# Optimization experiments

Hardware: AMD Instinct MI355X
Metric: run time of the kernel (lower is better)

## Reference

```python
import jax, jax.numpy as jnp
from jax import lax
import numpy as np

B, IMG_H, IMG_W = 8, 256, 512
NUM_CLASSES, P = 20, 32
SCALE, TOPK, IOU_THR = 32.0, 100, 0.5


def conv2d(x, w, b, stride=1, pad=1):
    y = lax.conv_general_dilated(x, w, (stride, stride), [(pad, pad), (pad, pad)],
                                 dimension_numbers=('NCHW', 'OIHW', 'NCHW'))
    return y + b[None, :, None, None]


def bilinear_resize(img, out_h, out_w):
    # img: [..., H, W]; torch F.interpolate(mode='bilinear', align_corners=False)
    H, W = img.shape[-2], img.shape[-1]
    def idx_w(n_in, n_out):
        src = (jnp.arange(n_out, dtype=jnp.float32) + 0.5) * (n_in / n_out) - 0.5
        src = jnp.clip(src, 0.0, n_in - 1)
        i0 = jnp.floor(src).astype(jnp.int32)
        i1 = jnp.minimum(i0 + 1, n_in - 1)
        return i0, i1, src - i0.astype(jnp.float32)
    y0, y1, wy = idx_w(H, out_h)
    x0, x1, wx = idx_w(W, out_w)
    top = img[..., y0, :] * (1.0 - wy)[:, None] + img[..., y1, :] * wy[:, None]
    return top[..., x0] * (1.0 - wx) + top[..., x1] * wx


def generate_anchors(fh, fw):
    ys = (jnp.arange(fh, dtype=jnp.float32) + 0.5) * (IMG_H / fh)
    xs = (jnp.arange(fw, dtype=jnp.float32) + 0.5) * (IMG_W / fw)
    cy, cx = jnp.meshgrid(ys, xs, indexing='ij')
    h = SCALE / 2
    return jnp.stack([cx - h, cy - h, cx + h, cy + h], -1).reshape(-1, 4)


def delta_to_boxes(anchors, deltas):
    a_c = (anchors[:, :2] + anchors[:, 2:]) / 2
    a_wh = anchors[:, 2:] - anchors[:, :2]
    pc = a_c + deltas[..., :2] * a_wh
    pwh = a_wh * jnp.exp(deltas[..., 2:])
    return jnp.concatenate([pc - pwh / 2, pc + pwh / 2], -1)


def nms_single(boxes, scores, labels):
    # torchvision batched_nms: offset boxes per label, greedy NMS, return kept idxs
    N = boxes.shape[0]
    off = labels.astype(boxes.dtype) * (jnp.max(boxes) + 1.0)
    b = boxes + off[:, None]
    order = jnp.argsort(-scores)
    bs = b[order]
    area = (bs[:, 2] - bs[:, 0]) * (bs[:, 3] - bs[:, 1])
    lt = jnp.maximum(bs[:, None, :2], bs[None, :, :2])
    rb = jnp.minimum(bs[:, None, 2:], bs[None, :, 2:])
    wh = jnp.clip(rb - lt, 0.0)
    inter = wh[..., 0] * wh[..., 1]
    iou = inter / (area[:, None] + area[None, :] - inter + 1e-9)
    idxs = jnp.arange(N)
    def body(i, suppressed):
        keep_i = jnp.logical_not(suppressed[i])
        row = (iou[i] > IOU_THR) & (idxs > i)
        return jnp.where(keep_i, suppressed | row, suppressed)
    suppressed = lax.fori_loop(0, N, body, jnp.zeros(N, bool))
    keep_mask = ~suppressed
    rank = jnp.cumsum(keep_mask) - 1
    slots = jnp.where(keep_mask & (rank < TOPK), rank, TOPK)
    out = jnp.full(TOPK + 1, -1, jnp.int32).at[slots].set(order.astype(jnp.int32))
    return out[:TOPK]


def setup_inputs():
    key = jax.random.key(0)
    ks = jax.random.split(key, 17)
    def cw(k, o, i, kh, kw_):
        return jax.random.normal(k, (o, i, kh, kw_), jnp.float32) / np.sqrt(i * kh * kw_)
    return {
        'images': jax.random.normal(ks[0], (B, 3, IMG_H, IMG_W), jnp.float32),
        'w1': cw(ks[1], 64, 3, 3, 3),   'b1': jnp.zeros(64, jnp.float32),
        'w2': cw(ks[2], 128, 64, 3, 3), 'b2': jnp.zeros(128, jnp.float32),
        'w3': cw(ks[3], 256, 128, 3, 3),'b3': jnp.zeros(256, jnp.float32),
        'pw1': cw(ks[4], 256, 256, 3, 3), 'pb1': jnp.zeros(256, jnp.float32),
        'pw2': cw(ks[5], P, 256, 1, 1),   'pb2': jnp.zeros(P, jnp.float32),
        'cw_': cw(ks[6], NUM_CLASSES + 1, 256, 3, 3), 'cb': jnp.zeros(NUM_CLASSES + 1, jnp.float32),
        'bw': cw(ks[7], 4, 256, 3, 3),  'bb': jnp.zeros(4, jnp.float32),
        'kw': cw(ks[8], P, 256, 3, 3),  'kb': jnp.zeros(P, jnp.float32),
    }


def reference(images, w1, b1, w2, b2, w3, b3, pw1, pb1, pw2, pb2, cw_, cb, bw, bb, kw, kb):
    x = jax.nn.relu(conv2d(images, w1, b1, stride=2))
    x = jax.nn.relu(conv2d(x, w2, b2, stride=2))
    feat = jax.nn.relu(conv2d(x, w3, b3, stride=2))          # [B,256,32,64]
    proto = conv2d(jax.nn.relu(conv2d(feat, pw1, pb1)), pw2, pb2, pad=0)  # [B,P,32,64]
    fh, fw = feat.shape[2], feat.shape[3]
    def head(w, b, c):
        return conv2d(feat, w, b).transpose(0, 2, 3, 1).reshape(B, -1, c)
    cls = head(cw_, cb, NUM_CLASSES + 1)     # [B,N,C+1]
    box = head(bw, bb, 4)                    # [B,N,4]
    coef = head(kw, kb, P)                   # [B,N,P]
    anchors = generate_anchors(fh, fw)       # [N,4]
    probs = jax.nn.softmax(cls, -1)[..., :-1]
    scores = probs.max(-1)
    labels = probs.argmax(-1).astype(jnp.int32)
    boxes = delta_to_boxes(anchors, box)     # [B,N,4]
    keep = jax.vmap(nms_single)(boxes, scores, labels)   # [B,100], -1 pad
    valid = keep >= 0
    ki = jnp.clip(keep, 0)
    take = lambda a: jnp.take_along_axis(a, ki[..., None] if a.ndim == 3 else ki, axis=1)
    boxes_k = take(boxes) * valid[..., None]
    scores_k = take(scores) * valid
    labels_k = jnp.where(valid, take(labels), 0)
    coef_k = jnp.take_along_axis(coef, ki[..., None], axis=1)   # [B,100,P]
    m = jax.nn.sigmoid(jnp.einsum('bkp,bphw->bkhw', coef_k, proto))
    masks = bilinear_resize(m, IMG_H, IMG_W) > 0.5
    masks = masks & valid[..., None, None]
    return boxes_k, scores_k, labels_k, masks, valid
```

## Files before the change

kernel.cpp:

```cpp
#include <hip/hip_runtime.h>
#include <hip/hip_bf16.h>
#include <math.h>

#define BB 8
#define NCLS 21
#define NANCH 2048
#define TOPK_N 100

static const size_t OFF_X1HI = 0;
static const size_t OFF_X1LO = 34344960;
static const size_t OFF_X2HI = 68689920;
static const size_t OFF_X2LO = 86261760;
static const size_t OFF_FTHI = 103833600;
static const size_t OFF_FTLO = 113025024;
static const size_t OFF_WT1  = 122216448;
static const size_t OFF_A2H  = 122223616;
static const size_t OFF_A2L  = 122371072;
static const size_t OFF_A3H  = 122518528;
static const size_t OFF_A3L  = 123108352;
static const size_t OFF_AHH  = 123698176;
static const size_t OFF_AHL  = 123993088;
static const size_t OFF_AP1H = 124288000;
static const size_t OFF_AP1L = 125467648;
static const size_t OFF_WTP2 = 126647296;
static const size_t OFF_BH   = 126680064;
static const size_t OFF_HOUT = 126680576;
static const size_t OFF_P1   = 130874880;
static const size_t OFF_PROTO= 147652096;
static const size_t OFF_BOXES= 149749248;
static const size_t OFF_SCORES=150011392;
static const size_t OFF_LABELS=150076928;
static const size_t OFF_ORDER= 150142464;
static const size_t OFF_SB   = 150208000;
static const size_t OFF_IOU  = 150470144;
static const size_t OFF_KEEP = 154664448;
static const size_t OFF_MAXB = 154668032;

static const size_t OUT_BOXES  = 0;
static const size_t OUT_SCORES = 3200;
static const size_t OUT_LABELS = 4000;
static const size_t OUT_MASKS  = 4800;
static const size_t OUT_VALID  = 104862400;

typedef __attribute__((ext_vector_type(8))) short bf16x8;
typedef __attribute__((ext_vector_type(4))) float f32x4;

__device__ __forceinline__ unsigned encf(float f){
  unsigned u = __float_as_uint(f);
  return (u & 0x80000000u) ? ~u : (u | 0x80000000u);
}
__device__ __forceinline__ float decf(unsigned u){
  unsigned b = (u & 0x80000000u) ? (u & 0x7fffffffu) : ~u;
  return __uint_as_float(b);
}
__device__ __forceinline__ short f2bf(float f){
  __hip_bfloat16 h = __float2bfloat16(f);
  return *(short*)&h;
}
__device__ __forceinline__ float bf2f(short h){
  return __uint_as_float(((unsigned)(unsigned short)h) << 16);
}

__global__ void halok3(short* __restrict__ x1hi, short* __restrict__ x1lo,
                       short* __restrict__ x2hi, short* __restrict__ x2lo,
                       short* __restrict__ fthi, short* __restrict__ ftlo,
                       unsigned* __restrict__ maxb){
  int i = blockIdx.x*256 + threadIdx.x;
  if (i < BB) maxb[i] = 0u;
  short *hi, *lo; int Hp, Wp, cell, bg;
  if (i < 49408){
    hi=x1hi; lo=x1lo; Hp=130; Wp=258; cell = i % 772; bg = i / 772;
  } else if (i < 99072){
    int j = i - 49408; hi=x2hi; lo=x2lo; Hp=66; Wp=130; cell = j % 388; bg = j / 388;
  } else if (i < 149248){
    int j = i - 99072; hi=fthi; lo=ftlo; Hp=34; Wp=66; cell = j % 196; bg = j / 196;
  } else return;
  int y, x;
  if (cell < Wp)        { y = 0;      x = cell; }
  else if (cell < 2*Wp) { y = Hp-1;   x = cell - Wp; }
  else { int r = cell - 2*Wp; y = 1 + (r>>1); x = (r&1) ? (Wp-1) : 0; }
  size_t ad = (((size_t)bg*Hp + y)*Wp + x)*8;
  bf16x8 z = (bf16x8){0,0,0,0,0,0,0,0};
  *(bf16x8*)(hi + ad) = z;
  *(bf16x8*)(lo + ad) = z;
}

template<int CIN,int COUT,int KK>
__device__ __forceinline__ void packw_body(int i, const float* __restrict__ w,
                                           float* __restrict__ wT){
  if (i >= CIN*KK*COUT) return;
  int co = i % COUT; int r = i / COUT;
  int ci = r / KK,  k = r % KK;
  wT[i] = w[(co*CIN + ci)*KK + k];
}

template<int CIN,int COUT>
__device__ __forceinline__ void packA_body(int i, const float* __restrict__ w,
                                           short* __restrict__ Ahi, short* __restrict__ Alo){
  constexpr int K = CIN*9;
  constexpr int KS = K/32;
  if (i >= COUT*K) return;
  int sub  = i & 7;
  int lane = (i >> 3) & 63;
  int rest = i >> 9;
  int ks = rest % KS;
  int mt = rest / KS;
  int m = mt*16 + (lane & 15);
  int k = ks*32 + (lane >> 4)*8 + sub;
  int tap = k / CIN, ci = k - tap*CIN;
  float v = w[(m*CIN + ci)*9 + tap];
  short h = f2bf(v);
  Ahi[i] = h;
  Alo[i] = f2bf(v - bf2f(h));
}

__device__ __forceinline__ void packAh_body(int i,
    const float* __restrict__ cw, const float* __restrict__ bw,
    const float* __restrict__ kw, const float* __restrict__ cb,
    const float* __restrict__ bb, const float* __restrict__ kb,
    short* __restrict__ Ahi, short* __restrict__ Alo, float* __restrict__ bh){
  if (i < 64){
    float v = 0.f;
    if (i < 21) v = cb[i]; else if (i < 25) v = bb[i-21]; else if (i < 57) v = kb[i-25];
    bh[i] = v;
  }
  if (i >= 64*2304) return;
  constexpr int KS = 72;
  int sub  = i & 7;
  int lane = (i >> 3) & 63;
  int rest = i >> 9;
  int ks = rest % KS;
  int mt = rest / KS;
  int m = mt*16 + (lane & 15);
  int k = ks*32 + (lane >> 4)*8 + sub;
  int tap = k >> 8, ci = k & 255;
  float v = 0.f;
  if (m < 21)      v = cw[(m*256 + ci)*9 + tap];
  else if (m < 25) v = bw[((m-21)*256 + ci)*9 + tap];
  else if (m < 57) v = kw[((m-25)*256 + ci)*9 + tap];
  short h = f2bf(v);
  Ahi[i] = h;
  Alo[i] = f2bf(v - bf2f(h));
}

__global__ void packall(const float* __restrict__ w1, float* __restrict__ wT1,
                        const float* __restrict__ w2, short* __restrict__ a2h, short* __restrict__ a2l,
                        const float* __restrict__ w3, short* __restrict__ a3h, short* __restrict__ a3l,
                        const float* __restrict__ pw1, short* __restrict__ ap1h, short* __restrict__ ap1l,
                        const float* __restrict__ cw, const float* __restrict__ bw,
                        const float* __restrict__ kw, const float* __restrict__ cb,
                        const float* __restrict__ bb, const float* __restrict__ kb,
                        short* __restrict__ ahh, short* __restrict__ ahl, float* __restrict__ bh,
                        const float* __restrict__ pw2, float* __restrict__ wTp2){
  int blk = blockIdx.x, t = threadIdx.x;
  if (blk < 288)        packA_body<64,128>(blk*256+t, w2, a2h, a2l);
  else if (blk < 1440)  packA_body<128,256>((blk-288)*256+t, w3, a3h, a3l);
  else if (blk < 3744)  packA_body<256,256>((blk-1440)*256+t, pw1, ap1h, ap1l);
  else if (blk < 4320)  packAh_body((blk-3744)*256+t, cw,bw,kw,cb,bb,kb, ahh,ahl,bh);
  else if (blk < 4327)  packw_body<3,64,9>((blk-4320)*256+t, w1, wT1);
  else                  packw_body<256,32,1>((blk-4327)*256+t, pw2, wTp2);
}

__global__ __launch_bounds__(256) void conv1k(const float* __restrict__ img,
    const float* __restrict__ wT, const float* __restrict__ bias,
    short* __restrict__ x1hi, short* __restrict__ x1lo){
  const int b   = blockIdx.z;
  const int co0 = blockIdx.y * 16;
  const int g   = blockIdx.x*256 + threadIdx.x;
  const int y  = g >> 7;
  const int x0 = (g & 127) << 1;

  float acc[16][2];
#pragma unroll
  for (int c=0;c<16;c++){
    float bv = bias[co0+c];
    acc[c][0] = bv; acc[c][1] = bv;
  }
  int   off[3][5];
  float msk[3][5];
#pragma unroll
  for (int kh=0;kh<3;kh++){
    int iy = y*2 - 1 + kh;
    bool okr = (iy >= 0) && (iy < 256);
    int ro = okr ? iy*512 : 0;
#pragma unroll
    for (int t=0;t<5;t++){
      int col = x0*2 - 1 + t;
      bool ok = okr && (col >= 0) && (col < 512);
      off[kh][t] = ok ? (ro + col) : 0;
      msk[kh][t] = ok ? 1.f : 0.f;
    }
  }
  const float* inb = img + (size_t)b*3*256*512;
  for (int ci=0; ci<3; ci++){
    const float* inc = inb + (size_t)ci*256*512;
    float v[3][5];
#pragma unroll
    for (int kh=0;kh<3;kh++)
#pragma unroll
      for (int t=0;t<5;t++)
        v[kh][t] = inc[off[kh][t]] * msk[kh][t];
    const float* wp = wT + ci*9*64 + co0;
#pragma unroll
    for (int kh=0;kh<3;kh++)
#pragma unroll
    for (int kw=0;kw<3;kw++){
      const float* wq = wp + (kh*3+kw)*64;
#pragma unroll
      for (int c=0;c<16;c++){
        float wv = wq[c];
        acc[c][0] = fmaf(wv, v[kh][2*0+kw], acc[c][0]);
        acc[c][1] = fmaf(wv, v[kh][2*1+kw], acc[c][1]);
      }
    }
  }
#pragma unroll
  for (int s=0;s<2;s++){
    short hv[16] __attribute__((aligned(16)));
    short lv[16] __attribute__((aligned(16)));
#pragma unroll
    for (int c=0;c<16;c++){
      float r = fmaxf(acc[c][s], 0.f);
      short h = f2bf(r);
      hv[c] = h;
      lv[c] = f2bf(r - bf2f(h));
    }
#pragma unroll
    for (int g2=0; g2<2; g2++){
      size_t ad = (((size_t)(b*8 + (co0>>3) + g2)*130 + (y+1))*258 + (x0+s+1))*8;
      *(bf16x8*)(x1hi + ad) = *(bf16x8*)(hv + g2*8);
      *(bf16x8*)(x1lo + ad) = *(bf16x8*)(lv + g2*8);
    }
  }
}

template<int CIN,int K,int M,int MW,int NW,int S,int IPH,int IPW,int NXB,
         bool SPLIT,bool STAGELO,int EMODE,int OPH,int OPW>
__global__ __launch_bounds__(NW*64) void cgemm_row(
    const short* __restrict__ Ahi, const short* __restrict__ Alo,
    const short* __restrict__ Bhi, const short* __restrict__ Blo,
    const float* __restrict__ bias, float* __restrict__ outf,
    short* __restrict__ outhi, short* __restrict__ outlo){
  static_assert(CIN % 32 == 0, "CIN must be multiple of 32");
  constexpr int NT = 64*32;
  constexpr int KS = K/32;
  constexpr int CG = CIN/8;
  constexpr int SW  = 64*S + 2;
  constexpr int SWP = (S==2) ? (SW/2 + 1) : SW;
  constexpr int PARS = (S==2) ? 2 : 1;
  constexpr int LOOFF = CG*PARS*SWP*8;
  constexpr int BUFS = (SPLIT && STAGELO) ? 2 : 1;
  __shared__ __align__(16) short sB[BUFS*LOOFF];

  const int b    = blockIdx.z;
  const int oy   = blockIdx.x / NXB;
  const int xb   = (blockIdx.x % NXB) * 64;
  const int wave = threadIdx.x >> 6;
  const int lane = threadIdx.x & 63;
  const int lm = lane & 15, lq = lane >> 4;
  const int m0 = (blockIdx.y * NW + wave) * (MW*16);
  const int tid = threadIdx.x;

  f32x4 acc[MW][4];
#pragma unroll
  for (int i=0;i<MW;i++)
#pragma unroll
    for (int j=0;j<4;j++) acc[i][j] = (f32x4){0.f,0.f,0.f,0.f};

  const short* Ah_l = Ahi + (size_t)lane*8;
  const short* Al_l = Alo + (size_t)lane*8;
  const int mt0 = m0 >> 4;
  const size_t plane = (size_t)IPH*IPW;
  const short* Bl0 = Blo + ((size_t)b*CG + lq)*plane*8;

#pragma unroll 1
  for (int dy=0; dy<3; dy++){
    const int iy = oy*S + dy;
    __syncthreads();
    {
      const short* srch = Bhi + (((size_t)b*CG*IPH + iy)*IPW + (size_t)(xb*S))*8;
      for (int c = tid; c < CG*SW; c += NW*64){
        int g = c / SW, p = c - g*SW;
        int dst = (S==2) ? ((g*2 + (p&1))*SWP + (p>>1)) : (g*SW + p);
        *(bf16x8*)(&sB[(size_t)dst*8]) =
          *(const bf16x8*)(srch + ((size_t)g*plane + p)*8);
      }
      if constexpr (SPLIT && STAGELO){
        const short* srcl = Blo + (((size_t)b*CG*IPH + iy)*IPW + (size_t)(xb*S))*8;
        for (int c = tid; c < CG*SW; c += NW*64){
          int g = c / SW, p = c - g*SW;
          int dst = (S==2) ? ((g*2 + (p&1))*SWP + (p>>1)) : (g*SW + p);
          *(bf16x8*)(&sB[LOOFF + (size_t)dst*8]) =
            *(const bf16x8*)(srcl + ((size_t)g*plane + p)*8);
        }
      }
    }
    __syncthreads();
#pragma unroll
    for (int dx=0; dx<3; dx++){
      const int tap = dy*3 + dx;
      const int ksb = tap*(CIN/32);
      for (int kc=0; kc<CIN; kc+=32){
        const int ks = ksb + (kc>>5);
        int ra[4];
#pragma unroll
        for (int j=0;j<4;j++){
          int pc = (j*16 + lm)*S + dx;
          ra[j] = (S==2) ? ((((kc>>3) + lq)*2 + (pc&1))*SWP + (pc>>1))
                         : (((kc>>3) + lq)*SW + pc);
        }
        bf16x8 ah[MW], bh_[4];
#pragma unroll
        for (int i=0;i<MW;i++)
          ah[i] = *(const bf16x8*)(Ah_l + ((size_t)(mt0+i)*KS + ks)*512);
#pragma unroll
        for (int j=0;j<4;j++)
          bh_[j] = *(const bf16x8*)(&sB[(size_t)ra[j]*8]);
        if constexpr (SPLIT){
          bf16x8 al[MW], bl_[4];
#pragma unroll
          for (int i=0;i<MW;i++)
            al[i] = *(const bf16x8*)(Al_l + ((size_t)(mt0+i)*KS + ks)*512);
          if constexpr (STAGELO){
#pragma unroll
            for (int j=0;j<4;j++)
              bl_[j] = *(const bf16x8*)(&sB[LOOFF + (size_t)ra[j]*8]);
          } else {
#pragma unroll
            for (int j=0;j<4;j++){
              size_t pix = (size_t)iy*IPW + (size_t)((xb + j*16 + lm)*S + dx);
              bl_[j] = *(const bf16x8*)(Bl0 + ((size_t)(kc>>3)*plane + pix)*8);
            }
          }
#pragma unroll
          for (int j=0;j<4;j++)
#pragma unroll
            for (int i=0;i<MW;i++)
              acc[i][j] = __builtin_amdgcn_mfma_f32_16x16x32_bf16(ah[i], bh_[j], acc[i][j], 0,0,0);
#pragma unroll
          for (int j=0;j<4;j++)
#pragma unroll
            for (int i=0;i<MW;i++)
              acc[i][j] = __builtin_amdgcn_mfma_f32_16x16x32_bf16(ah[i], bl_[j], acc[i][j], 0,0,0);
#pragma unroll
          for (int j=0;j<4;j++)
#pragma unroll
            for (int i=0;i<MW;i++)
              acc[i][j] = __builtin_amdgcn_mfma_f32_16x16x32_bf16(al[i], bh_[j], acc[i][j], 0,0,0);
        } else {
#pragma unroll
          for (int j=0;j<4;j++)
#pragma unroll
            for (int i=0;i<MW;i++)
              acc[i][j] = __builtin_amdgcn_mfma_f32_16x16x32_bf16(ah[i], bh_[j], acc[i][j], 0,0,0);
        }
      }
    }
  }

#pragma unroll
  for (int i=0;i<MW;i++){
#pragma unroll
    for (int r=0;r<4;r++){
      const int m = m0 + i*16 + lq*4 + r;
      const float bv = bias[m];
      if constexpr (EMODE == 0){
#pragma unroll
        for (int j=0;j<4;j++){
          const int ox = xb + j*16 + lm;
          float v = fmaxf(acc[i][j][r] + bv, 0.f);
          short h = f2bf(v);
          short l = f2bf(v - bf2f(h));
          size_t ad = ((((size_t)(b*(M/8) + (m>>3))*OPH + (oy+1))*OPW + (ox+1)))*8 + (m&7);
          outhi[ad] = h;
          outlo[ad] = l;
        }
      } else {
        float* cp = outf + ((size_t)b*M + m)*NT + oy*64 + lm;
#pragma unroll
        for (int j=0;j<4;j++){
          float v = acc[i][j][r] + bv;
          if constexpr (EMODE == 2) v = fmaxf(v, 0.f);
          cp[j*16] = v;
        }
      }
    }
  }
}

__global__ __launch_bounds__(256) void headsdec(
    const short* __restrict__ Ahi, const short* __restrict__ Alo,
    const short* __restrict__ Bhi, const short* __restrict__ Blo,
    const float* __restrict__ bias, float* __restrict__ hout,
    float* __restrict__ boxes, float* __restrict__ scores,
    int* __restrict__ labels, unsigned* __restrict__ maxb){
  constexpr int KS = 72;
  constexpr int CG = 32;
  constexpr int SW = 66;
  constexpr int IPH = 34, IPW = 66;
  constexpr int LOOFF = CG*SW*8;
  __shared__ __align__(16) short sB[2*LOOFF];

  const int b  = blockIdx.z;
  const int oy = blockIdx.x;
  const int wave = threadIdx.x >> 6;
  const int lane = threadIdx.x & 63;
  const int lm = lane & 15, lq = lane >> 4;
  const int tid = threadIdx.x;

  f32x4 acc[4];
#pragma unroll
  for (int j=0;j<4;j++) acc[j] = (f32x4){0.f,0.f,0.f,0.f};

  const short* Ah_l = Ahi + (size_t)lane*8;
  const short* Al_l = Alo + (size_t)lane*8;
  const size_t plane = (size_t)IPH*IPW;

#pragma unroll 1
  for (int dy=0; dy<3; dy++){
    const int iy = oy + dy;
    __syncthreads();
    {
      const short* srch = Bhi + ((size_t)b*CG*IPH + iy)*IPW*8;
      const short* srcl = Blo + ((size_t)b*CG*IPH + iy)*IPW*8;
      for (int c = tid; c < CG*SW; c += 256){
        int g = c / SW, p = c - g*SW;
        *(bf16x8*)(&sB[(size_t)c*8]) =
          *(const bf16x8*)(srch + ((size_t)g*plane + p)*8);
        *(bf16x8*)(&sB[LOOFF + (size_t)c*8]) =
          *(const bf16x8*)(srcl + ((size_t)g*plane + p)*8);
      }
    }
    __syncthreads();
#pragma unroll
    for (int dx=0; dx<3; dx++){
      const int tap = dy*3 + dx;
      const int ksb = tap*8;
      for (int kc=0; kc<256; kc+=32){
        const int ks = ksb + (kc>>5);
        int ra[4];
#pragma unroll
        for (int j=0;j<4;j++) ra[j] = ((kc>>3) + lq)*SW + (j*16 + lm) + dx;
        bf16x8 bh_[4], bl_[4];
#pragma unroll
        for (int j=0;j<4;j++){
          bh_[j] = *(const bf16x8*)(&sB[(size_t)ra[j]*8]);
          bl_[j] = *(const bf16x8*)(&sB[LOOFF + (size_t)ra[j]*8]);
        }
        bf16x8 ah = *(const bf16x8*)(Ah_l + ((size_t)wave*KS + ks)*512);
        bf16x8 al = *(const bf16x8*)(Al_l + ((size_t)wave*KS + ks)*512);
#pragma unroll
        for (int j=0;j<4;j++)
          acc[j] = __builtin_amdgcn_mfma_f32_16x16x32_bf16(ah, bh_[j], acc[j], 0,0,0);
#pragma unroll
        for (int j=0;j<4;j++)
          acc[j] = __builtin_amdgcn_mfma_f32_16x16x32_bf16(ah, bl_[j], acc[j], 0,0,0);
#pragma unroll
        for (int j=0;j<4;j++)
          acc[j] = __builtin_amdgcn_mfma_f32_16x16x32_bf16(al, bh_[j], acc[j], 0,0,0);
      }
    }
  }

  __syncthreads();
  float* sF = (float*)sB;
#pragma unroll
  for (int r=0;r<4;r++){
    const int m = wave*16 + lq*4 + r;
    const float bv = bias[m];
    float* cp = hout + ((size_t)b*64 + m)*NANCH + oy*64 + lm;
#pragma unroll
    for (int j=0;j<4;j++){
      float v = acc[j][r] + bv;
      cp[j*16] = v;
      sF[m*68 + j*16 + lm] = v;
    }
  }
  __syncthreads();

  if (tid < 64){
    const int n = oy*64 + tid;
    float l[NCLS];
    float M = -1e30f;
#pragma unroll
    for (int c=0;c<NCLS;c++){ l[c] = sF[c*68 + tid]; M = fmaxf(M, l[c]); }
    float denom = 0.f;
#pragma unroll
    for (int c=0;c<NCLS;c++) denom += expf(l[c]-M);
    float best = -1.f; int bi = 0;
#pragma unroll
    for (int c=0;c<NCLS-1;c++){
      float e = expf(l[c]-M);
      if (e > best){ best = e; bi = c; }
    }
    scores[(size_t)b*NANCH + n] = best/denom;
    labels[(size_t)b*NANCH + n] = bi;

    float dxv = sF[21*68 + tid], dyv = sF[22*68 + tid];
    float dwv = sF[23*68 + tid], dhv = sF[24*68 + tid];
    const int yy = n >> 6, xx = n & 63;
    float cx = (xx+0.5f)*8.f, cy = (yy+0.5f)*8.f;
    float px = cx + dxv*32.f, py = cy + dyv*32.f;
    float pw = 32.f*expf(dwv), ph = 32.f*expf(dhv);
    float x1 = px - 0.5f*pw, y1 = py - 0.5f*ph;
    float x2 = px + 0.5f*pw, y2 = py + 0.5f*ph;
    float* bo = boxes + ((size_t)b*NANCH + n)*4;
    bo[0]=x1; bo[1]=y1; bo[2]=x2; bo[3]=y2;
    float mx = fmaxf(fmaxf(x1,y1), fmaxf(x2,y2));
#pragma unroll
    for (int off=32; off>0; off>>=1) mx = fmaxf(mx, __shfl_down(mx, off));
    if (tid == 0) atomicMax(maxb + b, encf(mx));
  }
}

__global__ __launch_bounds__(256) void pw2k2(const float* __restrict__ p1,
    const float* __restrict__ wT, const float* __restrict__ bias,
    float* __restrict__ proto){
  const int b  = blockIdx.y;
  const int sp = blockIdx.x*256 + threadIdx.x;
  float acc[32];
#pragma unroll
  for (int c=0;c<32;c++) acc[c] = bias[c];
  const float* pb = p1 + (size_t)b*256*NANCH + sp;
  for (int ci=0;ci<256;ci++){
    float v = pb[(size_t)ci*NANCH];
    const float* wq = wT + ci*32;
#pragma unroll
    for (int c=0;c<32;c++) acc[c] = fmaf(v, wq[c], acc[c]);
  }
#pragma unroll
  for (int c=0;c<32;c++)
    proto[((size_t)b*32 + c)*NANCH + sp] = acc[c];
}

__global__ void __launch_bounds__(1024) sortk(const float* __restrict__ scores,
                     const float* __restrict__ boxes, const int* __restrict__ labels,
                     const unsigned* __restrict__ maxb,
                     int* __restrict__ order, float* __restrict__ sb){
  __shared__ float sc[NANCH];
  __shared__ int   id[NANCH];
  const int b = blockIdx.x, t = threadIdx.x;
  for (int i=t;i<NANCH;i+=1024){ sc[i]=scores[(size_t)b*NANCH+i]; id[i]=i; }
  __syncthreads();
  for (int k=2;k<=NANCH;k<<=1){
    for (int j=k>>1;j>0;j>>=1){
      for (int i=t;i<NANCH;i+=1024){
        int ixj = i ^ j;
        if (ixj > i){
          float sa=sc[i], sb_=sc[ixj]; int ia=id[i], ib=id[ixj];
          bool dir = ((i & k) == 0);
          bool before_ba = (sb_ > sa) || (sb_ == sa && ib < ia);
          if (before_ba == dir){ sc[i]=sb_; sc[ixj]=sa; id[i]=ib; id[ixj]=ia; }
        }
      }
      __syncthreads();
    }
  }
  float mboff = decf(maxb[b]) + 1.0f;
  for (int r=t;r<NANCH;r+=1024){
    int o = id[r];
    order[(size_t)b*NANCH + r] = o;
    float off = (float)labels[(size_t)b*NANCH + o] * mboff;
    const float* bo = boxes + ((size_t)b*NANCH + o)*4;
    float* sp = sb + ((size_t)b*NANCH + r)*4;
    sp[0]=bo[0]+off; sp[1]=bo[1]+off; sp[2]=bo[2]+off; sp[3]=bo[3]+off;
  }
}

__global__ void ioumask(const float* __restrict__ sb, unsigned long long* __restrict__ iou){
  const int b = blockIdx.y;
  const int gid = blockIdx.x*blockDim.x + threadIdx.x;
  const int i = gid >> 5, w = gid & 31;
  const float* base = sb + (size_t)b*NANCH*4;
  unsigned long long bits = 0ull;
  const int j0 = w << 6;
  if (j0 + 63 > i){
    float x1=base[i*4], y1=base[i*4+1], x2=base[i*4+2], y2=base[i*4+3];
    float ai = (x2-x1)*(y2-y1);
    for (int jj=0;jj<64;jj++){
      int j = j0 + jj;
      if (j > i){
        float bx1=base[j*4], by1=base[j*4+1], bx2=base[j*4+2], by2=base[j*4+3];
        float lx=fmaxf(x1,bx1), ly=fmaxf(y1,by1);
        float rx=fminf(x2,bx2), ry=fminf(y2,by2);
        float ww=fmaxf(rx-lx,0.f), hh=fmaxf(ry-ly,0.f);
        float inter = ww*hh;
        float aj = (bx2-bx1)*(by2-by1);
        float v = inter/(ai + aj - inter + 1e-9f);
        if (v > 0.5f) bits |= (1ull << jj);
      }
    }
  }
  iou[((size_t)b*NANCH + i)*32 + w] = bits;
}

__global__ void nmsgather(const unsigned long long* __restrict__ iou,
                          const int* __restrict__ order,
                          const float* __restrict__ boxes, const float* __restrict__ scores,
                          const int* __restrict__ labels,
                          int* __restrict__ keep, float* __restrict__ out){
  const int b = blockIdx.x, lane = threadIdx.x;
  __shared__ int s_keep[TOPK_N];
  unsigned long long sup = 0ull;
  int k = 0, i = 0;
  while (k < TOPK_N){
    unsigned long long avail = (lane < 32) ? ~sup : 0ull;
    const int wi = i >> 6;
    if (lane < wi) avail = 0ull;
    else if (lane == wi) avail &= (~0ull) << (i & 63);
    unsigned long long ball = __ballot(avail != 0ull);
    if (!ball) break;
    int w0 = (int)__builtin_ctzll(ball);
    unsigned long long aw = __shfl(avail, w0);
    int b0 = (int)__builtin_ctzll(aw);
    i = (w0 << 6) + b0;
    int ov = order[(size_t)b*NANCH + i];
    if (lane == 0) s_keep[k] = ov;
    k++;
    unsigned long long row = (lane < 32) ? iou[((size_t)b*NANCH + i)*32 + lane] : 0ull;
    sup |= row;
    i++;
    if (i >= NANCH) break;
  }
  __syncthreads();
  for (int r = lane; r < TOPK_N; r += 64){
    int kv = (r < k) ? s_keep[r] : -1;
    keep[b*TOPK_N + r] = kv;
    float valid = (kv >= 0) ? 1.f : 0.f;
    int kc = (kv < 0) ? 0 : kv;
    const float* bo = boxes + ((size_t)b*NANCH + kc)*4;
#pragma unroll
    for (int c=0;c<4;c++) out[OUT_BOXES + ((size_t)b*TOPK_N + r)*4 + c] = bo[c]*valid;
    out[OUT_SCORES + b*TOPK_N + r] = scores[(size_t)b*NANCH + kc]*valid;
    out[OUT_LABELS + b*TOPK_N + r] = (kv >= 0) ? (float)labels[(size_t)b*NANCH + kc] : 0.f;
    out[OUT_VALID  + b*TOPK_N + r] = valid;
  }
}

__global__ __launch_bounds__(256) void maskresize(const int* __restrict__ keep,
    const float* __restrict__ hout, const float* __restrict__ proto,
    float* __restrict__ out){
  const int b = blockIdx.y, r = blockIdx.x;
  float* obase = out + OUT_MASKS + ((size_t)b*TOPK_N + r)*131072;
  int ki = keep[b*TOPK_N + r];
  if (ki < 0){
    float4 z = make_float4(0.f,0.f,0.f,0.f);
    for (int idx = threadIdx.x; idx < 32768; idx += 256)
      ((float4*)obase)[idx] = z;
    return;
  }
  __shared__ float cf[32];
  __shared__ float sm[NANCH];
  if (threadIdx.x < 32)
    cf[threadIdx.x] = hout[((size_t)b*64 + 25 + threadIdx.x)*NANCH + ki];
  __syncthreads();
  for (int s = threadIdx.x; s < NANCH; s += 256){
    float acc = 0.f;
#pragma unroll
    for (int p=0;p<32;p++) acc = fmaf(cf[p], proto[((size_t)b*32 + p)*NANCH + s], acc);
    sm[s] = 1.f/(1.f + expf(-acc));
  }
  __syncthreads();
  for (int pid = threadIdx.x; pid < 32768; pid += 256){
    const int y  = pid >> 7;
    const int x4 = (pid & 127) << 2;
    float sy = (y + 0.5f)*0.125f - 0.5f;
    sy = fminf(fmaxf(sy, 0.f), 31.f);
    int y0 = (int)floorf(sy);
    int y1 = min(y0+1, 31);
    float wy = sy - (float)y0;
    const float* r0 = sm + y0*64;
    const float* r1 = sm + y1*64;
    float res[4];
#pragma unroll
    for (int kk=0;kk<4;kk++){
      int x = x4 + kk;
      float sx = (x + 0.5f)*0.125f - 0.5f;
      sx = fminf(fmaxf(sx, 0.f), 63.f);
      int x0 = (int)floorf(sx);
      int x1 = min(x0+1, 63);
      float wx = sx - (float)x0;
      float t0 = r0[x0]*(1.f-wy) + r1[x0]*wy;
      float t1 = r0[x1]*(1.f-wy) + r1[x1]*wy;
      float v  = t0*(1.f-wx) + t1*wx;
      res[kk] = (v > 0.5f) ? 1.f : 0.f;
    }
    *(float4*)(obase + y*512 + x4) = make_float4(res[0], res[1], res[2], res[3]);
  }
}

extern "C" void kernel_launch(void* const* d_in, const int* in_sizes, int n_in,
                              void* d_out, int out_size, void* d_ws, size_t ws_size,
                              hipStream_t stream) {
  const float* images=(const float*)d_in[0];
  const float* w1=(const float*)d_in[1];  const float* b1=(const float*)d_in[2];
  const float* w2=(const float*)d_in[3];  const float* b2=(const float*)d_in[4];
  const float* w3=(const float*)d_in[5];  const float* b3=(const float*)d_in[6];
  const float* pw1=(const float*)d_in[7]; const float* pb1=(const float*)d_in[8];
  const float* pw2=(const float*)d_in[9]; const float* pb2=(const float*)d_in[10];
  const float* cw=(const float*)d_in[11]; const float* cb=(const float*)d_in[12];
  const float* bw=(const float*)d_in[13]; const float* bb=(const float*)d_in[14];
  const float* kw=(const float*)d_in[15]; const float* kb=(const float*)d_in[16];
  float* out = (float*)d_out;
  char* ws = (char*)d_ws;

  short* x1hi = (short*)(ws + OFF_X1HI);
  short* x1lo = (short*)(ws + OFF_X1LO);
  short* x2hi = (short*)(ws + OFF_X2HI);
  short* x2lo = (short*)(ws + OFF_X2LO);
  short* fthi = (short*)(ws + OFF_FTHI);
  short* ftlo = (short*)(ws + OFF_FTLO);
  float* wT1  = (float*)(ws + OFF_WT1);
  short* a2h  = (short*)(ws + OFF_A2H);
  short* a2l  = (short*)(ws + OFF_A2L);
  short* a3h  = (short*)(ws + OFF_A3H);
  short* a3l  = (short*)(ws + OFF_A3L);
  short* ahh  = (short*)(ws + OFF_AHH);
  short* ahl  = (short*)(ws + OFF_AHL);
  short* ap1h = (short*)(ws + OFF_AP1H);
  short* ap1l = (short*)(ws + OFF_AP1L);
  float* wTp2 = (float*)(ws + OFF_WTP2);
  float* bh   = (float*)(ws + OFF_BH);
  float* hout = (float*)(ws + OFF_HOUT);
  float* p1   = (float*)(ws + OFF_P1);
  float* proto= (float*)(ws + OFF_PROTO);
  float* boxes= (float*)(ws + OFF_BOXES);
  float* scores=(float*)(ws + OFF_SCORES);
  int*   labels=(int*)  (ws + OFF_LABELS);
  int*   order =(int*)  (ws + OFF_ORDER);
  float* sb   = (float*)(ws + OFF_SB);
  unsigned long long* iou = (unsigned long long*)(ws + OFF_IOU);
  int*   keep = (int*)  (ws + OFF_KEEP);
  unsigned* maxb = (unsigned*)(ws + OFF_MAXB);

  halok3<<<dim3(583), 256, 0, stream>>>(x1hi, x1lo, x2hi, x2lo, fthi, ftlo, maxb);

  packall<<<dim3(4359), 256, 0, stream>>>(w1, wT1, w2, a2h, a2l, w3, a3h, a3l,
                                          pw1, ap1h, ap1l, cw, bw, kw, cb, bb, kb,
                                          ahh, ahl, bh, pw2, wTp2);

  conv1k<<<dim3(64,4,BB), 256, 0, stream>>>(images, wT1, b1, x1hi, x1lo);

  cgemm_row<64,576,128,2,4,2,130,258,2,true,true,0,66,130>
      <<<dim3(128,1,BB), 256, 0, stream>>>(a2h, a2l, x1hi, x1lo, b2, nullptr, x2hi, x2lo);

  cgemm_row<128,1152,256,2,4,2,66,130,1,true,true,0,34,66>
      <<<dim3(32,2,BB), 256, 0, stream>>>(a3h, a3l, x2hi, x2lo, b3, nullptr, fthi, ftlo);

  headsdec<<<dim3(32,1,BB), 256, 0, stream>>>(ahh, ahl, fthi, ftlo, bh, hout,
                                              boxes, scores, labels, maxb);

  cgemm_row<256,2304,256,2,4,1,34,66,1,false,false,2,1,1>
      <<<dim3(32,2,BB), 256, 0, stream>>>(ap1h, ap1l, fthi, fthi, pb1, p1, nullptr, nullptr);

  pw2k2<<<dim3(8,BB), 256, 0, stream>>>(p1, wTp2, pb2, proto);

  sortk<<<dim3(BB), 1024, 0, stream>>>(scores, boxes, labels, maxb, order, sb);
  ioumask<<<dim3(256,BB), 256, 0, stream>>>(sb, iou);
  nmsgather<<<dim3(BB), 64, 0, stream>>>(iou, order, boxes, scores, labels, keep, out);

  maskresize<<<dim3(TOPK_N,BB), 256, 0, stream>>>(keep, hout, proto, out);
}
```

Before: 970.4 us.

## Prefetch next input row into registers while computing current row

Adds a register-staged prefetch to the row conv GEMM kernels and the heads kernel. The next dy row is loaded from global memory into registers before the MFMA loop over the current row, then written to LDS between barriers, so global load latency overlaps with compute. It is enabled for the third conv and the proto conv, and always for the heads kernel. The inner kc loop is also fully unrolled. This raises register pressure and may lower occupancy, particularly in the split hi/lo paths.

```diff
diff --git a/kernel.cpp b/kernel.cpp
--- a/kernel.cpp
+++ b/kernel.cpp
@@ -235,7 +235,7 @@
 }
 
 template<int CIN,int K,int M,int MW,int NW,int S,int IPH,int IPW,int NXB,
-         bool SPLIT,bool STAGELO,int EMODE,int OPH,int OPW>
+         bool SPLIT,bool STAGELO,bool STAGEREG,int EMODE,int OPH,int OPW>
 __global__ __launch_bounds__(NW*64) void cgemm_row(
     const short* __restrict__ Ahi, const short* __restrict__ Alo,
     const short* __restrict__ Bhi, const short* __restrict__ Blo,
@@ -250,6 +250,8 @@
   constexpr int PARS = (S==2) ? 2 : 1;
   constexpr int LOOFF = CG*PARS*SWP*8;
   constexpr int BUFS = (SPLIT && STAGELO) ? 2 : 1;
+  constexpr int NTH = NW*64;
+  constexpr int NLD = (CG*SW + NTH - 1)/NTH;
   __shared__ __align__(16) short sB[BUFS*LOOFF];
 
   const int b    = blockIdx.z;
@@ -273,33 +275,83 @@
   const size_t plane = (size_t)IPH*IPW;
   const short* Bl0 = Blo + ((size_t)b*CG + lq)*plane*8;
 
+  bf16x8 rh[STAGEREG ? NLD : 1];
+  bf16x8 rl[(STAGEREG && SPLIT && STAGELO) ? NLD : 1];
+
+  auto LOADS = [&](int iyv){
+    const short* srch = Bhi + (((size_t)b*CG*IPH + iyv)*IPW + (size_t)(xb*S))*8;
+#pragma unroll
+    for (int t=0;t<NLD;t++){
+      int c = tid + t*NTH;
+      if (c < CG*SW){
+        int g = c / SW, p = c - g*SW;
+        rh[t] = *(const bf16x8*)(srch + ((size_t)g*plane + p)*8);
+      }
+    }
+    if constexpr (SPLIT && STAGELO){
+      const short* srcl = Blo + (((size_t)b*CG*IPH + iyv)*IPW + (size_t)(xb*S))*8;
+#pragma unroll
+      for (int t=0;t<NLD;t++){
+        int c = tid + t*NTH;
+        if (c < CG*SW){
+          int g = c / SW, p = c - g*SW;
+          rl[t] = *(const bf16x8*)(srcl + ((size_t)g*plane + p)*8);
+        }
+      }
+    }
+  };
+  auto WRITES = [&](){
+#pragma unroll
+    for (int t=0;t<NLD;t++){
+      int c = tid + t*NTH;
+      if (c < CG*SW){
+        int g = c / SW, p = c - g*SW;
+        int dst = (S==2) ? ((g*2 + (p&1))*SWP + (p>>1)) : (g*SW + p);
+        *(bf16x8*)(&sB[(size_t)dst*8]) = rh[t];
+        if constexpr (SPLIT && STAGELO)
+          *(bf16x8*)(&sB[LOOFF + (size_t)dst*8]) = rl[t];
+      }
+    }
+  };
+
+  if constexpr (STAGEREG){
+    LOADS(oy*S);
+    WRITES();
+    __syncthreads();
+  }
+
 #pragma unroll 1
   for (int dy=0; dy<3; dy++){
     const int iy = oy*S + dy;
-    __syncthreads();
-    {
-      const short* srch = Bhi + (((size_t)b*CG*IPH + iy)*IPW + (size_t)(xb*S))*8;
-      for (int c = tid; c < CG*SW; c += NW*64){
-        int g = c / SW, p = c - g*SW;
-        int dst = (S==2) ? ((g*2 + (p&1))*SWP + (p>>1)) : (g*SW + p);
-        *(bf16x8*)(&sB[(size_t)dst*8]) =
-          *(const bf16x8*)(srch + ((size_t)g*plane + p)*8);
-      }
-      if constexpr (SPLIT && STAGELO){
-        const short* srcl = Blo + (((size_t)b*CG*IPH + iy)*IPW + (size_t)(xb*S))*8;
-        for (int c = tid; c < CG*SW; c += NW*64){
+    if constexpr (STAGEREG){
+      if (dy < 2) LOADS(oy*S + dy + 1);
+    } else {
+      __syncthreads();
+      {
+        const short* srch = Bhi + (((size_t)b*CG*IPH + iy)*IPW + (size_t)(xb*S))*8;
+        for (int c = tid; c < CG*SW; c += NTH){
           int g = c / SW, p = c - g*SW;
           int dst = (S==2) ? ((g*2 + (p&1))*SWP + (p>>1)) : (g*SW + p);
-          *(bf16x8*)(&sB[LOOFF + (size_t)dst*8]) =
-            *(const bf16x8*)(srcl + ((size_t)g*plane + p)*8);
+          *(bf16x8*)(&sB[(size_t)dst*8]) =
+            *(const bf16x8*)(srch + ((size_t)g*plane + p)*8);
         }
-      }
-    }
-    __syncthreads();
+        if constexpr (SPLIT && STAGELO){
+          const short* srcl = Blo + (((size_t)b*CG*IPH + iy)*IPW + (size_t)(xb*S))*8;
+          for (int c = tid; c < CG*SW; c += NTH){
+            int g = c / SW, p = c - g*SW;
+            int dst = (S==2) ? ((g*2 + (p&1))*SWP + (p>>1)) : (g*SW + p);
+            *(bf16x8*)(&sB[LOOFF + (size_t)dst*8]) =
+              *(const bf16x8*)(srcl + ((size_t)g*plane + p)*8);
+          }
+        }
+      }
+      __syncthreads();
+    }
 #pragma unroll
     for (int dx=0; dx<3; dx++){
       const int tap = dy*3 + dx;
       const int ksb = tap*(CIN/32);
+#pragma unroll
       for (int kc=0; kc<CIN; kc+=32){
         const int ks = ksb + (kc>>5);
         int ra[4];
@@ -354,6 +406,13 @@
             for (int i=0;i<MW;i++)
               acc[i][j] = __builtin_amdgcn_mfma_f32_16x16x32_bf16(ah[i], bh_[j], acc[i][j], 0,0,0);
         }
+      }
+    }
+    if constexpr (STAGEREG){
+      if (dy < 2){
+        __syncthreads();
+        WRITES();
+        __syncthreads();
       }
     }
   }
@@ -399,6 +458,7 @@
   constexpr int SW = 66;
   constexpr int IPH = 34, IPW = 66;
   constexpr int LOOFF = CG*SW*8;
+  constexpr int NLD = (CG*SW + 255)/256;
   __shared__ __align__(16) short sB[2*LOOFF];
 
   const int b  = blockIdx.z;
@@ -416,26 +476,43 @@
   const short* Al_l = Alo + (size_t)lane*8;
   const size_t plane = (size_t)IPH*IPW;
 
+  bf16x8 rh[NLD], rl[NLD];
+  auto HLOADS = [&](int iyv){
+    const short* srch = Bhi + ((size_t)b*CG*IPH + iyv)*IPW*8;
+    const short* srcl = Blo + ((size_t)b*CG*IPH + iyv)*IPW*8;
+#pragma unroll
+    for (int t=0;t<NLD;t++){
+      int c = tid + t*256;
+      if (c < CG*SW){
+        int g = c / SW, p = c - g*SW;
+        rh[t] = *(const bf16x8*)(srch + ((size_t)g*plane + p)*8);
+        rl[t] = *(const bf16x8*)(srcl + ((size_t)g*plane + p)*8);
+      }
+    }
+  };
+  auto HWRITES = [&](){
+#pragma unroll
+    for (int t=0;t<NLD;t++){
+      int c = tid + t*256;
+      if (c < CG*SW){
+        *(bf16x8*)(&sB[(size_t)c*8]) = rh[t];
+        *(bf16x8*)(&sB[LOOFF + (size_t)c*8]) = rl[t];
+      }
+    }
+  };
+
+  HLOADS(oy);
+  HWRITES();
+  __syncthreads();
+
 #pragma unroll 1
   for (int dy=0; dy<3; dy++){
-    const int iy = oy + dy;
-    __syncthreads();
-    {
-      const short* srch = Bhi + ((size_t)b*CG*IPH + iy)*IPW*8;
-      const short* srcl = Blo + ((size_t)b*CG*IPH + iy)*IPW*8;
-      for (int c = tid; c < CG*SW; c += 256){
-        int g = c / SW, p = c - g*SW;
-        *(bf16x8*)(&sB[(size_t)c*8]) =
-          *(const bf16x8*)(srch + ((size_t)g*plane + p)*8);
-        *(bf16x8*)(&sB[LOOFF + (size_t)c*8]) =
-          *(const bf16x8*)(srcl + ((size_t)g*plane + p)*8);
-      }
-    }
-    __syncthreads();
+    if (dy < 2) HLOADS(oy + dy + 1);
 #pragma unroll
     for (int dx=0; dx<3; dx++){
       const int tap = dy*3 + dx;
       const int ksb = tap*8;
+#pragma unroll
       for (int kc=0; kc<256; kc+=32){
         const int ks = ksb + (kc>>5);
         int ra[4];
@@ -459,6 +536,11 @@
         for (int j=0;j<4;j++)
           acc[j] = __builtin_amdgcn_mfma_f32_16x16x32_bf16(al, bh_[j], acc[j], 0,0,0);
       }
+    }
+    if (dy < 2){
+      __syncthreads();
+      HWRITES();
+      __syncthreads();
     }
   }
 
@@ -741,16 +823,16 @@
 
   conv1k<<<dim3(64,4,BB), 256, 0, stream>>>(images, wT1, b1, x1hi, x1lo);
 
-  cgemm_row<64,576,128,2,4,2,130,258,2,true,true,0,66,130>
+  cgemm_row<64,576,128,2,4,2,130,258,2,true,true,false,0,66,130>
       <<<dim3(128,1,BB), 256, 0, stream>>>(a2h, a2l, x1hi, x1lo, b2, nullptr, x2hi, x2lo);
 
-  cgemm_row<128,1152,256,2,4,2,66,130,1,true,true,0,34,66>
+  cgemm_row<128,1152,256,2,4,2,66,130,1,true,true,true,0,34,66>
       <<<dim3(32,2,BB), 256, 0, stream>>>(a3h, a3l, x2hi, x2lo, b3, nullptr, fthi, ftlo);
 
   headsdec<<<dim3(32,1,BB), 256, 0, stream>>>(ahh, ahl, fthi, ftlo, bh, hout,
                                               boxes, scores, labels, maxb);
 
-  cgemm_row<256,2304,256,2,4,1,34,66,1,false,false,2,1,1>
+  cgemm_row<256,2304,256,2,4,1,34,66,1,false,false,true,2,1,1>
       <<<dim3(32,2,BB), 256, 0, stream>>>(ap1h, ap1l, fthi, fthi, pb1, p1, nullptr, nullptr);
 
   pw2k2<<<dim3(8,BB), 256, 0, stream>>>(p1, wTp2, pb2, proto);
```

New measurement: 953.4 us. Within noise of the previous version (-1.8%).
